# Optimization experiments

Hardware: AMD Instinct MI355X
Metric: run time of the kernel (lower is better)

Reference implementation:

```python
import jax, jax.numpy as jnp
import numpy as np

B, N, E = 262144, 14, 12
THRESHOLD = 0.3


def setup_inputs() -> dict:
    key = jax.random.key(0)
    k1, k2 = jax.random.split(key)
    pos = jax.random.normal(k1, (B, N, 3), dtype=jnp.float32)
    rot = jax.random.normal(k2, (B, N, 9), dtype=jnp.float32)
    # two 7-node kinematic chains: left arm nodes 0..6, right arm nodes 7..13
    left = np.stack([np.arange(6), np.arange(1, 7)])
    right = np.stack([np.arange(7, 13), np.arange(8, 14)])
    edge_index = jnp.asarray(np.concatenate([left, right], axis=1), dtype=jnp.int32)  # [2, 12]
    ee_mask = jnp.zeros((N, 1), dtype=bool).at[6, 0].set(True).at[13, 0].set(True)
    return {"pos": pos, "rot": rot, "edge_index": edge_index, "ee_mask": ee_mask}


def _capsule_capsule_dist_square(p0, p1, q0, q1):
    # p*: [B, K, 3] left capsules (vary along axis j), q*: [B, K, 3] right capsules (vary along axis i)
    dp = p1 - p0                                  # [B, K, 3]
    dq = q1 - q0                                  # [B, K, 3]
    diff0 = p0[:, None, :, :] - q0[:, :, None, :]  # [B, K(i=q), K(j=p), 3]
    a = jnp.sum(dp * dp, -1)[:, None, :]          # [B, 1, K]
    c = jnp.sum(dq * dq, -1)[:, :, None]          # [B, K, 1]
    b = jnp.einsum('bjd,bid->bij', dp, dq)        # [B, K, K]
    d = jnp.sum(dp[:, None, :, :] * diff0, -1)
    e = jnp.sum(dq[:, :, None, :] * diff0, -1)
    det = a * c - b * b
    bte, ctd, ate, btd = b * e, c * d, a * e, b * d
    s = jnp.zeros_like(det)
    t = jnp.zeros_like(det)
    one = jnp.ones_like(det)
    s = jnp.where((det > 0) & (bte <= ctd) & (e <= 0) & (-d >= a), one, s)
    s = jnp.where((det > 0) & (bte <= ctd) & (e <= 0) & (-d < a) & (-d > 0), -d / a, s)
    t = jnp.where((det > 0) & (bte <= ctd) & (e > 0) & (e < c), e / c, t)
    s = jnp.where((det > 0) & (bte <= ctd) & (e > 0) & (e >= c) & (b - d >= a), one, s)
    s = jnp.where((det > 0) & (bte <= ctd) & (e > 0) & (e >= c) & (b - d < a) & (b - d > 0), (b - d) / a, s)
    t = jnp.where((det > 0) & (bte <= ctd) & (e > 0) & (e >= c), one, t)
    s = jnp.where((det > 0) & (bte > ctd) & (bte - ctd >= det) & (b + e <= 0) & (-d > 0) & (-d < a), -d / a, s)
    s = jnp.where((det > 0) & (bte > ctd) & (bte - ctd >= det) & (b + e <= 0) & (-d > 0) & (-d >= a), one, s)
    s = jnp.where((det > 0) & (bte > ctd) & (bte - ctd >= det) & (b + e > 0) & (b + e < c), one, s)
    t = jnp.where((det > 0) & (bte > ctd) & (bte - ctd >= det) & (b + e > 0) & (b + e < c), (b + e) / c, t)
    s = jnp.where((det > 0) & (bte > ctd) & (bte - ctd >= det) & (b + e > 0) & (b + e >= c) & (b - d > 0) & (b - d < a), (b - d) / a, s)
    s = jnp.where((det > 0) & (bte > ctd) & (bte - ctd >= det) & (b + e > 0) & (b + e >= c) & (b - d > 0) & (b - d >= a), one, s)
    t = jnp.where((det > 0) & (bte > ctd) & (bte - ctd >= det) & (b + e > 0) & (b + e >= c), one, t)
    s = jnp.where((det > 0) & (bte > ctd) & (bte - ctd < det) & (ate <= btd) & (-d > 0) & (-d >= a), one, s)
    s = jnp.where((det > 0) & (bte > ctd) & (bte - ctd < det) & (ate <= btd) & (-d > 0) & (-d < a), -d / a, s)
    s = jnp.where((det > 0) & (bte > ctd) & (bte - ctd < det) & (ate > btd) & (ate - btd >= det) & (b - d > 0) & (b - d >= a), one, s)
    s = jnp.where((det > 0) & (bte > ctd) & (bte - ctd < det) & (ate > btd) & (ate - btd >= det) & (b - d > 0) & (b - d < a), (b - d) / a, s)
    t = jnp.where((det > 0) & (bte > ctd) & (bte - ctd < det) & (ate > btd) & (ate - btd >= det), one, t)
    s = jnp.where((det > 0) & (bte > ctd) & (bte - ctd < det) & (ate > btd) & (ate - btd < det), (bte - ctd) / det, s)
    t = jnp.where((det > 0) & (bte > ctd) & (bte - ctd < det) & (ate > btd) & (ate - btd < det), (ate - btd) / det, t)
    s = jnp.where((det <= 0) & (e <= 0) & (-d > 0) & (-d >= a), one, s)
    s = jnp.where((det <= 0) & (e <= 0) & (-d > 0) & (-d < a), -d / a, s)
    s = jnp.where((det <= 0) & (e > 0) & (e >= c) & (b - d > 0) & (b - d >= a), one, s)
    s = jnp.where((det <= 0) & (e > 0) & (e >= c) & (b - d > 0) & (b - d < a), (b - d) / a, s)
    t = jnp.where((det <= 0) & (e > 0) & (e >= c), one, t)
    t = jnp.where((det <= 0) & (e > 0) & (e < c), e / c, t)
    # original code detaches s and t before forming w
    s = jax.lax.stop_gradient(s)
    t = jax.lax.stop_gradient(t)
    w = diff0 + s[..., None] * dp[:, None, :, :] - t[..., None] * dq[:, :, None, :]
    return jnp.sum(w * w, -1)  # [B, K, K]


def reference(pos, rot, edge_index, ee_mask):
    bsz, n_nodes = pos.shape[0], pos.shape[1]
    n_edges = edge_index.shape[1]
    half = n_edges // 2
    p0 = pos[:, edge_index[0]]  # [B, E, 3]
    p1 = pos[:, edge_index[1]]
    l_p0, r_p0 = p0[:, :half], p0[:, half:]
    l_p1, r_p1 = p1[:, :half], p1[:, half:]
    # exactly 2 end-effectors (left, right) marked in ee_mask
    ee_idx = jnp.nonzero(ee_mask[:, 0], size=2)[0]
    ee_pos = pos[:, ee_idx]                         # [B, 2, 3]  (left, right)
    ee_rot = rot[:, ee_idx].reshape(bsz, 2, 3, 3)   # [B, 2, 3, 3]
    offset = jnp.array([0.0, 0.0, 0.2], dtype=pos.dtype)
    hand_pos = jnp.einsum('beij,j->bei', ee_rot, offset) + ee_pos  # [B, 2, 3]
    l_p0 = jnp.concatenate([l_p0, ee_pos[:, 0:1]], axis=1)   # [B, E/2+1, 3]
    l_p1 = jnp.concatenate([l_p1, hand_pos[:, 0:1]], axis=1)
    r_p0 = jnp.concatenate([r_p0, ee_pos[:, 1:2]], axis=1)
    r_p1 = jnp.concatenate([r_p1, hand_pos[:, 1:2]], axis=1)
    dist_square = _capsule_capsule_dist_square(l_p0, l_p1, r_p0, r_p1)  # [B, 7, 7]
    mask = (dist_square < 0.1 ** 2) & (dist_square > 0)
    special = (dist_square[:, 6, 6] > THRESHOLD ** 2) & (dist_square[:, 6, 6] > 0)
    mask = mask.at[:, 6, 6].set(special)
    loss = jnp.sum(jnp.where(mask, jnp.exp(-dist_square), jnp.zeros_like(dist_square))) / bsz
    return loss
```

## Files before the change

### kernel.cpp

```cpp
#include <hip/hip_runtime.h>


__device__ __forceinline__ float rcpf(float x) { return __builtin_amdgcn_rcpf(x); }
__device__ __forceinline__ float clamp01(float x) {
    return __builtin_amdgcn_fmed3f(x, 0.0f, 1.0f);
}

__device__ __forceinline__ float cap_dist2(
    float px0, float py0, float pz0, float px1, float py1, float pz1,
    float qx0, float qy0, float qz0, float qx1, float qy1, float qz1)
{
    const float dpx = px1 - px0, dpy = py1 - py0, dpz = pz1 - pz0;
    const float dqx = qx1 - qx0, dqy = qy1 - qy0, dqz = qz1 - qz0;
    const float rx  = px0 - qx0, ry  = py0 - qy0, rz  = pz0 - qz0;

    const float a = dpx*dpx + dpy*dpy + dpz*dpz;
    const float c = dqx*dqx + dqy*dqy + dqz*dqz;
    const float b = dpx*dqx + dpy*dqy + dpz*dqz;
    const float d = dpx*rx + dpy*ry + dpz*rz;
    const float e = dqx*rx + dqy*ry + dqz*rz;
    const float det = a*c - b*b;

    const float rcp_a = rcpf(a);
    const float rcp_c = rcpf(c);

    const float f  = b*e - c*d;
    const float s0 = (det > 0.0f) ? clamp01(f * rcpf(det)) : 0.0f;

    const float tn = b*s0 + e;
    const float t  = clamp01(tn * rcp_c);

    const float sA = clamp01(-d * rcp_a);
    const float sB = clamp01((b - d) * rcp_a);
    const float s  = (tn < 0.0f) ? sA : ((tn > c) ? sB : s0);

    const float wx = rx + s*dpx - t*dqx;
    const float wy = ry + s*dpy - t*dqy;
    const float wz = rz + s*dpz - t*dqz;
    return wx*wx + wy*wy + wz*wz;
}

#define BT 256

__global__ __launch_bounds__(BT) void collision_loss_kernel(
    const float* __restrict__ pos,
    const float* __restrict__ rot,
    float* __restrict__ out)
{
    __shared__ float2 sbuf[4][64 * 21];
    __shared__ float wsum[4];

    const int tid  = threadIdx.x;
    const int lane = tid & 63;
    const int wave = tid >> 6;
    const int blockBase = blockIdx.x * BT;
    const int slabBase  = blockBase + wave * 64;

    float2* slab = sbuf[wave];

    const float2* g2 = reinterpret_cast<const float2*>(pos + (size_t)slabBase * 42);
    float2 ld[21];
    #pragma unroll
    for (int k = 0; k < 21; ++k) ld[k] = g2[k * 64 + lane];

    const float* rb = rot + (size_t)(slabBase + lane) * 126;
    const float r6x = rb[ 56], r6y = rb[ 59], r6z = rb[ 62];
    const float rdx = rb[119], rdy = rb[122], rdz = rb[125];

    #pragma unroll
    for (int k = 0; k < 21; ++k) slab[k * 64 + lane] = ld[k];

    const float2* m2 = slab + (size_t)lane * 21;
    const float2 u0  = m2[0],  u1  = m2[1],  u2  = m2[2],  u3  = m2[3];
    const float2 u4  = m2[4],  u5  = m2[5],  u6  = m2[6],  u7  = m2[7];
    const float2 u8  = m2[8],  u9  = m2[9],  u10 = m2[10];
    const float2 u19 = m2[19], u20 = m2[20];

    const float n0x=u0.x,  n0y=u0.y,  n0z=u1.x;
    const float n1x=u1.y,  n1y=u2.x,  n1z=u2.y;
    const float n2x=u3.x,  n2y=u3.y,  n2z=u4.x;
    const float n3x=u4.y,  n3y=u5.x,  n3z=u5.y;
    const float n4x=u6.x,  n4y=u6.y,  n4z=u7.x;
    const float n5x=u7.y,  n5y=u8.x,  n5z=u8.y;
    const float n6x=u9.x,  n6y=u9.y,  n6z=u10.x;
    const float n13x=u19.y, n13y=u20.x, n13z=u20.y;

    const float hlx = n6x  + 0.2f * r6x;
    const float hly = n6y  + 0.2f * r6y;
    const float hlz = n6z  + 0.2f * r6z;
    const float hrx = n13x + 0.2f * rdx;
    const float hry = n13y + 0.2f * rdy;
    const float hrz = n13z + 0.2f * rdz;

    float sum0 = 0.0f, sum1 = 0.0f;

    auto acc = [&](float& s_, float p0x, float p0y, float p0z,
                   float p1x, float p1y, float p1z,
                   float q0x, float q0y, float q0z,
                   float q1x, float q1y, float q1z, bool special) {
        const float d2 = cap_dist2(p0x,p0y,p0z, p1x,p1y,p1z,
                                   q0x,q0y,q0z, q1x,q1y,q1z);
        const bool m = special ? (d2 > 0.09f)
                               : ((d2 < 0.01f) && (d2 > 0.0f));
        s_ += m ? __expf(-d2) : 0.0f;
    };

    #define LROW(QX0,QY0,QZ0,QX1,QY1,QZ1,SP)                                  \
        acc(sum0, n0x,n0y,n0z, n1x,n1y,n1z, QX0,QY0,QZ0, QX1,QY1,QZ1, false); \
        acc(sum1, n1x,n1y,n1z, n2x,n2y,n2z, QX0,QY0,QZ0, QX1,QY1,QZ1, false); \
        acc(sum0, n2x,n2y,n2z, n3x,n3y,n3z, QX0,QY0,QZ0, QX1,QY1,QZ1, false); \
        acc(sum1, n3x,n3y,n3z, n4x,n4y,n4z, QX0,QY0,QZ0, QX1,QY1,QZ1, false); \
        acc(sum0, n4x,n4y,n4z, n5x,n5y,n5z, QX0,QY0,QZ0, QX1,QY1,QZ1, false); \
        acc(sum1, n5x,n5y,n5z, n6x,n6y,n6z, QX0,QY0,QZ0, QX1,QY1,QZ1, false); \
        acc(sum0, n6x,n6y,n6z, hlx,hly,hlz, QX0,QY0,QZ0, QX1,QY1,QZ1, SP);

    const float* sf = reinterpret_cast<const float*>(slab) + (size_t)lane * 42;
    #pragma clang loop unroll(disable)
    for (int i = 0; i < 6; ++i) {
        const int f0 = 21 + 3 * i;
        const float q0x = sf[f0    ], q0y = sf[f0 + 1], q0z = sf[f0 + 2];
        const float q1x = sf[f0 + 3], q1y = sf[f0 + 4], q1z = sf[f0 + 5];
        LROW(q0x,q0y,q0z, q1x,q1y,q1z, false)
    }

    LROW(n13x,n13y,n13z, hrx,hry,hrz, true)
    #undef LROW

    float sum = sum0 + sum1;

    #pragma unroll
    for (int off = 32; off > 0; off >>= 1)
        sum += __shfl_down(sum, off, 64);
    if (lane == 0) wsum[wave] = sum;
    __syncthreads();
    if (tid == 0) {
        atomicAdd(out, (wsum[0] + wsum[1] + wsum[2] + wsum[3])
                       * (1.0f / 262144.0f));
    }
}

extern "C" void kernel_launch(void* const* d_in, const int* in_sizes, int n_in,
                              void* d_out, int out_size, void* d_ws, size_t ws_size,
                              hipStream_t stream) {
    const float* pos = (const float*)d_in[0];
    const float* rot = (const float*)d_in[1];
    float* out = (float*)d_out;

    const int B = in_sizes[0] / 42;
    hipMemsetAsync(out, 0, sizeof(float), stream);

    collision_loss_kernel<<<B / BT, BT, 0, stream>>>(pos, rot, out);
}
```

Before: 214.7 us.

## Split each batch row's capsule pairs across two waves with block-wide float4 staging

```diff
diff --git a/kernel.cpp b/kernel.cpp
--- a/kernel.cpp
+++ b/kernel.cpp
@@ -42,39 +42,38 @@
 
 #define BT 256
 
-__global__ __launch_bounds__(BT) void collision_loss_kernel(
+__global__ __launch_bounds__(BT, 8) void collision_loss_kernel(
     const float* __restrict__ pos,
     const float* __restrict__ rot,
     float* __restrict__ out)
 {
-    __shared__ float2 sbuf[4][64 * 21];
+    __shared__ float4 sb4[1344];
     __shared__ float wsum[4];
 
-    const int tid  = threadIdx.x;
-    const int lane = tid & 63;
-    const int wave = tid >> 6;
-    const int blockBase = blockIdx.x * BT;
-    const int slabBase  = blockBase + wave * 64;
+    const int tid     = threadIdx.x;
+    const int lane    = tid & 63;
+    const int wave    = tid >> 6;
+    const int slabIdx = tid >> 7;
+    const int s       = (tid >> 6) & 1;
+    const int r       = tid & 63;
 
-    float2* slab = sbuf[wave];
+    const float4* g4 = reinterpret_cast<const float4*>(pos) + (size_t)blockIdx.x * 1344;
+    #pragma unroll
+    for (int k = 0; k < 5; ++k) sb4[k * 256 + tid] = g4[k * 256 + tid];
+    if (tid < 64) sb4[1280 + tid] = g4[1280 + tid];
 
-    const float2* g2 = reinterpret_cast<const float2*>(pos + (size_t)slabBase * 42);
-    float2 ld[21];
-    #pragma unroll
-    for (int k = 0; k < 21; ++k) ld[k] = g2[k * 64 + lane];
+    const int myRow = blockIdx.x * 128 + slabIdx * 64 + r;
+    const float* rb = rot + (size_t)myRow * 126;
+    const float r6x = rb[56], r6y = rb[59], r6z = rb[62];
 
-    const float* rb = rot + (size_t)(slabBase + lane) * 126;
-    const float r6x = rb[ 56], r6y = rb[ 59], r6z = rb[ 62];
-    const float rdx = rb[119], rdy = rb[122], rdz = rb[125];
+    __syncthreads();
 
-    #pragma unroll
-    for (int k = 0; k < 21; ++k) slab[k * 64 + lane] = ld[k];
-
-    const float2* m2 = slab + (size_t)lane * 21;
-    const float2 u0  = m2[0],  u1  = m2[1],  u2  = m2[2],  u3  = m2[3];
-    const float2 u4  = m2[4],  u5  = m2[5],  u6  = m2[6],  u7  = m2[7];
-    const float2 u8  = m2[8],  u9  = m2[9],  u10 = m2[10];
-    const float2 u19 = m2[19], u20 = m2[20];
+    const float* sf = reinterpret_cast<const float*>(sb4)
+                      + (size_t)(slabIdx * 64 + r) * 42;
+    const float2* m2 = reinterpret_cast<const float2*>(sf);
+    const float2 u0 = m2[0], u1 = m2[1], u2 = m2[2], u3 = m2[3], u4 = m2[4];
+    const float2 u5 = m2[5], u6 = m2[6], u7 = m2[7], u8 = m2[8], u9 = m2[9];
+    const float2 u10 = m2[10];
 
     const float n0x=u0.x,  n0y=u0.y,  n0z=u1.x;
     const float n1x=u1.y,  n1y=u2.x,  n1z=u2.y;
@@ -83,14 +82,10 @@
     const float n4x=u6.x,  n4y=u6.y,  n4z=u7.x;
     const float n5x=u7.y,  n5y=u8.x,  n5z=u8.y;
     const float n6x=u9.x,  n6y=u9.y,  n6z=u10.x;
-    const float n13x=u19.y, n13y=u20.x, n13z=u20.y;
 
-    const float hlx = n6x  + 0.2f * r6x;
-    const float hly = n6y  + 0.2f * r6y;
-    const float hlz = n6z  + 0.2f * r6z;
-    const float hrx = n13x + 0.2f * rdx;
-    const float hry = n13y + 0.2f * rdy;
-    const float hrz = n13z + 0.2f * rdz;
+    const float hlx = n6x + 0.2f * r6x;
+    const float hly = n6y + 0.2f * r6y;
+    const float hlz = n6z + 0.2f * r6z;
 
     float sum0 = 0.0f, sum1 = 0.0f;
 
@@ -114,16 +109,24 @@
         acc(sum1, n5x,n5y,n5z, n6x,n6y,n6z, QX0,QY0,QZ0, QX1,QY1,QZ1, false); \
         acc(sum0, n6x,n6y,n6z, hlx,hly,hlz, QX0,QY0,QZ0, QX1,QY1,QZ1, SP);
 
-    const float* sf = reinterpret_cast<const float*>(slab) + (size_t)lane * 42;
+    const int iLo = s ? 4 : 0;
+    const int iHi = s ? 6 : 4;
     #pragma clang loop unroll(disable)
-    for (int i = 0; i < 6; ++i) {
+    for (int i = iLo; i < iHi; ++i) {
         const int f0 = 21 + 3 * i;
         const float q0x = sf[f0    ], q0y = sf[f0 + 1], q0z = sf[f0 + 2];
         const float q1x = sf[f0 + 3], q1y = sf[f0 + 4], q1z = sf[f0 + 5];
         LROW(q0x,q0y,q0z, q1x,q1y,q1z, false)
     }
 
-    LROW(n13x,n13y,n13z, hrx,hry,hrz, true)
+    if (s) {
+        const float rdx = rb[119], rdy = rb[122], rdz = rb[125];
+        const float n13x = sf[39], n13y = sf[40], n13z = sf[41];
+        const float hrx = n13x + 0.2f * rdx;
+        const float hry = n13y + 0.2f * rdy;
+        const float hrz = n13z + 0.2f * rdz;
+        LROW(n13x,n13y,n13z, hrx,hry,hrz, true)
+    }
     #undef LROW
 
     float sum = sum0 + sum1;
@@ -149,5 +152,5 @@
     const int B = in_sizes[0] / 42;
     hipMemsetAsync(out, 0, sizeof(float), stream);
 
-    collision_loss_kernel<<<B / BT, BT, 0, stream>>>(pos, rot, out);
+    collision_loss_kernel<<<B / 128, BT, 0, stream>>>(pos, rot, out);
 }
```

Result: no change. 216.3 us (+0.7%).
